# Kernel optimization log

Measured on AMD Instinct MI355X. Metric: run time of the kernel, lower is better.

The kernel has to match this reference:

```python
import jax, jax.numpy as jnp
import numpy as np
from jax import lax


def conv_valid_relu(x, w, b):
    # NHWC valid conv, stride 1, + bias + relu (matches keras Conv2D(..., activation='relu'))
    y = lax.conv_general_dilated(x, w, (1, 1), 'VALID',
                                 dimension_numbers=('NHWC', 'HWIO', 'NHWC'))
    return jax.nn.relu(y + b)


def maxpool2(x):
    # keras MaxPooling2D(): pool 2x2, stride 2, VALID
    return lax.reduce_window(x, -jnp.inf, lax.max, (1, 2, 2, 1), (1, 2, 2, 1), 'VALID')


def affine_bilinear(img, theta):
    # img: [H, W, C]; theta: [6] = (a0..a5).
    # tf.raw_ops.ImageProjectiveTransformV3 semantics (a6=a7=0):
    #   x_in = a0*x_out + a1*y_out + a2;  y_in = a3*x_out + a4*y_out + a5
    # BILINEAR interp; each of the 4 neighbor reads returns fill_value(=0) if out of bounds.
    H, W, C = img.shape
    a0, a1, a2, a3, a4, a5 = theta
    ys, xs = jnp.meshgrid(jnp.arange(H, dtype=img.dtype),
                          jnp.arange(W, dtype=img.dtype), indexing='ij')
    xq = a0 * xs + a1 * ys + a2  # [H, W]
    yq = a3 * xs + a4 * ys + a5
    x0 = jnp.floor(xq)
    y0 = jnp.floor(yq)
    dx = xq - x0
    dy = yq - y0

    def read(yi, xi):
        valid = (yi >= 0) & (yi <= H - 1) & (xi >= 0) & (xi <= W - 1)
        yc = jnp.clip(yi, 0, H - 1).astype(jnp.int32)
        xc = jnp.clip(xi, 0, W - 1).astype(jnp.int32)
        v = img[yc, xc]  # gather -> [H, W, C]
        return jnp.where(valid[..., None], v, jnp.zeros((), img.dtype))

    v00 = read(y0, x0)
    v01 = read(y0, x0 + 1)
    v10 = read(y0 + 1, x0)
    v11 = read(y0 + 1, x0 + 1)
    top = v00 * (1 - dx)[..., None] + v01 * dx[..., None]
    bot = v10 * (1 - dx)[..., None] + v11 * dx[..., None]
    return top * (1 - dy)[..., None] + bot * dy[..., None]


def reference(x, conv1_w, conv1_b, conv2_w, conv2_b, fc_w, fc_b):
    y = conv_valid_relu(x, conv1_w, conv1_b)   # [B,218,218,8]
    y = maxpool2(y)                            # [B,109,109,8]
    y = conv_valid_relu(y, conv2_w, conv2_b)   # [B,105,105,10]
    y = maxpool2(y)                            # [B,52,52,10]
    feat = y.reshape(y.shape[0], -1)           # row-major HWC flatten == keras Flatten
    theta = feat @ fc_w + fc_b                 # [B,6]
    return jax.vmap(affine_bilinear)(x, theta)


def setup_inputs() -> dict:
    key = jax.random.key(0)
    ks = jax.random.split(key, 6)
    B, H, W, C = 64, 224, 224, 3
    flat_dim = 52 * 52 * 10  # from 224 -> conv7 -> pool -> conv5 -> pool
    x = jax.random.normal(ks[0], (B, H, W, C), dtype=jnp.float32)
    conv1_w = jax.random.normal(ks[1], (7, 7, 3, 8), dtype=jnp.float32) * 0.05
    conv1_b = jnp.zeros((8,), jnp.float32)
    conv2_w = jax.random.normal(ks[2], (5, 5, 8, 10), dtype=jnp.float32) * 0.05
    conv2_b = jnp.zeros((10,), jnp.float32)
    # keras init: kernel zeros, bias = identity affine. Add tiny noise to kernel so the
    # predicted transform actually varies per image (exercises the resampler).
    fc_w = jax.random.normal(ks[3], (flat_dim, 6), dtype=jnp.float32) * 1e-4
    fc_b = jnp.array([1.0, 0.0, 0.0, 0.0, 1.0, 0.0], dtype=jnp.float32)
    return {"x": x, "conv1_w": conv1_w, "conv1_b": conv1_b,
            "conv2_w": conv2_w, "conv2_b": conv2_b, "fc_w": fc_w, "fc_b": fc_b}
```

## Files before the change

### kernel.cpp

```cpp
#include <hip/hip_runtime.h>
#include <math.h>

#define BATCH 64
#define HI 224
#define WI 224
#define P1H 109
#define P1W 109
#define P2H 52
#define P2W 52

typedef _Float16 f16;
typedef _Float16 f16x4 __attribute__((ext_vector_type(4)));
typedef _Float16 f16x8 __attribute__((ext_vector_type(8)));
typedef float    f32x4 __attribute__((ext_vector_type(4)));

#define MFMA16F(a,b,c) __builtin_amdgcn_mfma_f32_16x16x32_f16((a),(b),(c),0,0,0)

#define PROWS 4
#define NROWG 28
#define SROWS 14
#define ROWSH 896
#define STOT  (SROWS*ROWSH)
#define SPAD  12576
__global__ __launch_bounds__(256) void conv1_kernel(
    const float* __restrict__ x, const float* __restrict__ w1,
    const float* __restrict__ b1,
    f16* __restrict__ p1)
{
    __shared__ f16 smem[SPAD + 7*16*32];
    f16* sh_a = smem;
    f16* sh_b = smem + SPAD;

    const int tid  = threadIdx.x;
    const int lane = tid & 63;
    const int wave = tid >> 6;
    const int bph  = blockIdx.x;
    const int b    = blockIdx.y;
    const int ph0  = PROWS*bph;
    const int ir0  = 2*ph0;

    for (int i = tid; i < 7*16*32; i += 256) sh_b[i] = (f16)0.f;
    __syncthreads();

    for (int i = tid; i < 1176; i += 256) {
        const float v = w1[i];
        const int co = i & 7;
        const int t3 = i >> 3;
        const int ci = t3 % 3;
        const int kk = t3 / 3;
        const int kh = kk / 7;
        const int kw = kk - kh*7;
        sh_b[(kh*16 + co)*32 + kw*4 + ci] = (f16)v;
    }

    for (int u = wave; u < 25; u += 4) {
        const int q = u*512 + lane*8;
        if (q >= SPAD) continue;
        const int row  = q / ROWSH;
        const int rem  = q - row*ROWSH;
        const int col0 = rem >> 2;
        const int ira  = ir0 + row;
        float f0=0.f,f1=0.f,f2=0.f,f3=0.f,f4=0.f,f5=0.f;
        if (q < STOT && ira < HI) {
            const float* src = x + ((size_t)(b*HI + ira)*WI + col0)*3;
            const float2 a = *(const float2*)(src);
            const float2 c = *(const float2*)(src+2);
            const float2 e = *(const float2*)(src+4);
            f0=a.x; f1=a.y; f2=c.x; f3=c.y; f4=e.x; f5=e.y;
        }
        f16x8 hv;
        hv[0]=(f16)f0; hv[1]=(f16)f1; hv[2]=(f16)f2; hv[3]=(f16)0.f;
        hv[4]=(f16)f3; hv[5]=(f16)f4; hv[6]=(f16)f5; hv[7]=(f16)0.f;
        *(f16x8*)(sh_a + q) = hv;
    }
    __syncthreads();

    const int n16 = lane & 15;
    const int g   = lane >> 4;

    f16x8 bw[7];
#pragma unroll
    for (int kh = 0; kh < 7; ++kh)
        bw[kh] = *(const f16x8*)(sh_b + (kh*16 + n16)*32 + g*8);
    const float bias = b1[n16 & 7];

    for (int t = wave; t < 14; t += 4) {
        const int abase = (t*16 + n16)*4 + g*8;
        f32x4 acc[8];
#pragma unroll
        for (int cr = 0; cr < 8; ++cr) acc[cr] = (f32x4){0.f,0.f,0.f,0.f};

#pragma unroll
        for (int ir = 0; ir < SROWS; ++ir) {
            const int sb = ir*ROWSH + abase;
            const int klo = (ir > 7) ? (ir-7) : 0;
            const int khi = (ir < 6) ? ir : 6;
            const f16x4 h0 = *(const f16x4*)(sh_a + sb);
            const f16x4 h1 = *(const f16x4*)(sh_a + sb + 4);
            const f16x8 ah = __builtin_shufflevector(h0,h1,0,1,2,3,4,5,6,7);
#pragma unroll
            for (int kh = klo; kh <= khi; ++kh)
                acc[ir-kh] = MFMA16F(ah, bw[kh], acc[ir-kh]);
        }

        if (n16 < 8) {
#pragma unroll
            for (int pr = 0; pr < PROWS; ++pr) {
                const int ph = ph0 + pr;
                if (ph >= P1H) break;
#pragma unroll
                for (int q = 0; q < 2; ++q) {
                    const int pc = t*8 + 2*g + q;
                    if (pc < P1W) {
                        float m = fmaxf(fmaxf(acc[2*pr][2*q], acc[2*pr][2*q+1]),
                                        fmaxf(acc[2*pr+1][2*q], acc[2*pr+1][2*q+1]));
                        m = fmaxf(m + bias, 0.f);
                        const size_t oi = ((size_t)((b*P1H + ph)*P1W) + pc)*8 + n16;
                        p1[oi] = (f16)m;
                    }
                }
            }
        }
    }
}

#define C2A 6144
__global__ __launch_bounds__(256) void conv2_kernel(
    const f16* __restrict__ p1,
    const float* __restrict__ w2, const float* __restrict__ b2,
    float* __restrict__ p2)
{
    __shared__ f16 smem[C2A + 16*224];
    f16* sh_a = smem;
    f16* sh_b = smem + C2A;

    const int tid = threadIdx.x;
    const int ph  = blockIdx.x;
    const int b   = blockIdx.y;

    for (int i = tid; i < 16*224; i += 256) sh_b[i] = (f16)0.f;
    for (int i = tid; i < C2A - 5232; i += 256) sh_a[5232 + i] = (f16)0.f;
    __syncthreads();

    for (int i = tid; i < 2000; i += 256) {
        const float v = w2[i];
        const int kh = i / 400;
        int rem = i - kh*400;
        const int kw = rem / 80;
        rem -= kw*80;
        const int ci = rem / 10;
        const int co = rem - ci*10;
        sh_b[co*224 + kh*40 + kw*8 + ci] = (f16)v;
    }

    const size_t gbase = ((size_t)b*P1H + 2*ph) * (P1W*8);
    const ulong2* gsrc = (const ulong2*)(p1 + gbase);
    ulong2* gdst = (ulong2*)sh_a;
    for (int c = tid; c < 654; c += 256) gdst[c] = gsrc[c];
    __syncthreads();

    const int lane = tid & 63;
    const int wave = tid >> 6;
    const int n16  = lane & 15;
    const int g    = lane >> 4;

    f16x8 bh[7];
#pragma unroll
    for (int j = 0; j < 7; ++j)
        bh[j] = *(const f16x8*)(sh_b + n16*224 + j*32 + g*8);
    const float bias = (n16 < 10) ? b2[n16] : 0.f;

    int koff[7];
#pragma unroll
    for (int j = 0; j < 7; ++j) {
        const int chunk = 4*j + g;
        const int kh = chunk / 5;
        const int kw = chunk - kh*5;
        koff[j] = kh*872 + kw*8;
    }

    for (int t = wave; t < 7; t += 4) {
        const int c0 = t*16;
        const int pbase = (c0 + n16)*8;
        float res[2][4];
#pragma unroll
        for (int ro = 0; ro < 2; ++ro) {
            f32x4 accA = {0.f,0.f,0.f,0.f};
            f32x4 accB = {0.f,0.f,0.f,0.f};
            const int rb = ro*872 + pbase;
#pragma unroll
            for (int j = 0; j < 7; ++j) {
                const int si = rb + koff[j];
                const f16x8 ah = *(const f16x8*)(sh_a + si);
                if (j & 1) accB = MFMA16F(ah, bh[j], accB);
                else       accA = MFMA16F(ah, bh[j], accA);
            }
#pragma unroll
            for (int r = 0; r < 4; ++r) res[ro][r] = accA[r] + accB[r];
        }
        if (n16 < 10) {
#pragma unroll
            for (int q = 0; q < 2; ++q) {
                const int pc = (c0 >> 1) + 2*g + q;
                if (pc < P2W) {
                    float m = fmaxf(fmaxf(res[0][2*q], res[0][2*q+1]),
                                    fmaxf(res[1][2*q], res[1][2*q+1]));
                    p2[((size_t)((b*P2H + ph)*P2W) + pc)*10 + n16] = fmaxf(m + bias, 0.f);
                }
            }
        }
    }
}

__global__ __launch_bounds__(256) void fcA_kernel(
    const float* __restrict__ p2, const float* __restrict__ fw,
    float* __restrict__ partial)
{
    const int s = blockIdx.x;
    const int b = blockIdx.y;
    const int base = s * 3380;
    const float* f = p2 + (size_t)b*27040;
    float acc[6] = {0.f,0.f,0.f,0.f,0.f,0.f};
    for (int i = threadIdx.x; i < 3380; i += 256) {
        const float v = f[base + i];
        const float* wp = fw + (size_t)(base + i)*6;
#pragma unroll
        for (int k = 0; k < 6; ++k) acc[k] = fmaf(v, wp[k], acc[k]);
    }
    __shared__ float red[4][6];
#pragma unroll
    for (int k = 0; k < 6; ++k) {
        float v = acc[k];
        for (int off = 32; off > 0; off >>= 1) v += __shfl_down(v, off);
        if ((threadIdx.x & 63) == 0) red[threadIdx.x >> 6][k] = v;
    }
    __syncthreads();
    if (threadIdx.x < 6) {
        const int k = threadIdx.x;
        partial[(b*8 + s)*6 + k] = red[0][k] + red[1][k] + red[2][k] + red[3][k];
    }
}

__global__ __launch_bounds__(384) void fcB_kernel(
    const float* __restrict__ partial, const float* __restrict__ fb,
    float* __restrict__ theta)
{
    const int t = threadIdx.x;
    const int b = t / 6, k = t - b*6;
    float s = fb[k];
#pragma unroll
    for (int j = 0; j < 8; ++j) s += partial[(b*8 + j)*6 + k];
    theta[b*6 + k] = s;
}

__global__ __launch_bounds__(256) void resample_kernel(
    const float* __restrict__ x, const float* __restrict__ theta,
    float* __restrict__ out)
{
    const int idx = blockIdx.x * 256 + threadIdx.x;
    const int total = BATCH * HI * WI;
    if (idx >= total) return;
    const int b   = idx / (HI*WI);
    const int pix = idx - b * (HI*WI);
    const int yo  = pix / WI;
    const int xo  = pix - yo * WI;

    const float* t = theta + b*6;
    const float a0 = t[0], a1 = t[1], a2 = t[2], a3 = t[3], a4 = t[4], a5 = t[5];

    const float fx = (float)xo, fy = (float)yo;
    const float xq = a0*fx + a1*fy + a2;
    const float yq = a3*fx + a4*fy + a5;
    const float x0f = floorf(xq), y0f = floorf(yq);
    const float dx = xq - x0f, dy = yq - y0f;
    const int x0 = (int)x0f, y0 = (int)y0f;

    const float* img = x + (size_t)b * (HI*WI*3);

    const int x1 = x0 + 1, y1 = y0 + 1;
    const bool vx0 = (x0 >= 0) && (x0 <= WI-1);
    const bool vx1 = (x1 >= 0) && (x1 <= WI-1);
    const bool vy0 = (y0 >= 0) && (y0 <= HI-1);
    const bool vy1 = (y1 >= 0) && (y1 <= HI-1);
    const int xc0 = min(max(x0, 0), WI-1);
    const int xc1 = min(max(x1, 0), WI-1);
    const int yc0 = min(max(y0, 0), HI-1);
    const int yc1 = min(max(y1, 0), HI-1);
    const float* p00 = img + (size_t)(yc0*WI + xc0)*3;
    const float* p01 = img + (size_t)(yc0*WI + xc1)*3;
    const float* p10 = img + (size_t)(yc1*WI + xc0)*3;
    const float* p11 = img + (size_t)(yc1*WI + xc1)*3;
    const float m00 = (vy0 && vx0) ? 1.f : 0.f;
    const float m01 = (vy0 && vx1) ? 1.f : 0.f;
    const float m10 = (vy1 && vx0) ? 1.f : 0.f;
    const float m11 = (vy1 && vx1) ? 1.f : 0.f;

    float* op = out + (size_t)idx * 3;
#pragma unroll
    for (int c = 0; c < 3; ++c) {
        const float v00 = m00 * p00[c];
        const float v01 = m01 * p01[c];
        const float v10 = m10 * p10[c];
        const float v11 = m11 * p11[c];
        const float top = v00 * (1.f - dx) + v01 * dx;
        const float bot = v10 * (1.f - dx) + v11 * dx;
        op[c] = top * (1.f - dy) + bot * dy;
    }
}

extern "C" void kernel_launch(void* const* d_in, const int* in_sizes, int n_in,
                              void* d_out, int out_size, void* d_ws, size_t ws_size,
                              hipStream_t stream) {
    const float* x   = (const float*)d_in[0];
    const float* w1  = (const float*)d_in[1];
    const float* b1  = (const float*)d_in[2];
    const float* w2  = (const float*)d_in[3];
    const float* b2  = (const float*)d_in[4];
    const float* fw  = (const float*)d_in[5];
    const float* fb  = (const float*)d_in[6];
    float* out = (float*)d_out;

    char* ws = (char*)d_ws;
    f16*  p1      = (f16*)ws;
    float* p2     = (float*)(ws + 12166144);
    float* partial= (float*)(ws + 19088384);
    float* th     = (float*)(ws + 19100672);

    conv1_kernel<<<dim3(NROWG, BATCH), 256, 0, stream>>>(x, w1, b1, p1);
    conv2_kernel<<<dim3(P2H, BATCH), 256, 0, stream>>>(p1, w2, b2, p2);
    fcA_kernel<<<dim3(8, BATCH), 256, 0, stream>>>(p2, fw, partial);
    fcB_kernel<<<dim3(1), 384, 0, stream>>>(partial, fb, th);

    const int total_pix = BATCH * HI * WI;
    resample_kernel<<<dim3((total_pix + 255)/256), 256, 0, stream>>>(x, th, out);
}
```

Measured before the change: 76.76 us.

## Pack two conv row offsets into MFMA N dimension and merge FC kernels

Conv1 now fills the unused upper 8 output columns of each 16-wide MFMA weight tile with the same weights shifted by one kernel row. Each accumulator then computes two adjacent conv rows at once, which roughly halves the MFMA count, and the vertical pool max is taken with a cross-lane shuffle. The two-stage FC reduction is also folded into one kernel per batch, removing a launch at the cost of less parallelism per image.

```diff
diff --git a/kernel.cpp b/kernel.cpp
--- a/kernel.cpp
+++ b/kernel.cpp
@@ -22,12 +22,13 @@
 #define ROWSH 896
 #define STOT  (SROWS*ROWSH)
 #define SPAD  12576
+#define NBVAR 8
 __global__ __launch_bounds__(256) void conv1_kernel(
     const float* __restrict__ x, const float* __restrict__ w1,
     const float* __restrict__ b1,
     f16* __restrict__ p1)
 {
-    __shared__ f16 smem[SPAD + 7*16*32];
+    __shared__ f16 smem[SPAD + NBVAR*16*32];
     f16* sh_a = smem;
     f16* sh_b = smem + SPAD;
 
@@ -39,7 +40,7 @@
     const int ph0  = PROWS*bph;
     const int ir0  = 2*ph0;
 
-    for (int i = tid; i < 7*16*32; i += 256) sh_b[i] = (f16)0.f;
+    for (int i = tid; i < NBVAR*16*32; i += 256) sh_b[i] = (f16)0.f;
     __syncthreads();
 
     for (int i = tid; i < 1176; i += 256) {
@@ -50,7 +51,9 @@
         const int kk = t3 / 3;
         const int kh = kk / 7;
         const int kw = kk - kh*7;
-        sh_b[(kh*16 + co)*32 + kw*4 + ci] = (f16)v;
+        const f16 val = (f16)v;
+        sh_b[(kh*16     + co  )*32 + kw*4 + ci] = val;
+        sh_b[((kh+1)*16 + co+8)*32 + kw*4 + ci] = val;
     }
 
     for (int u = wave; u < 25; u += 4) {
@@ -78,47 +81,46 @@
     const int n16 = lane & 15;
     const int g   = lane >> 4;
 
-    f16x8 bw[7];
-#pragma unroll
-    for (int kh = 0; kh < 7; ++kh)
-        bw[kh] = *(const f16x8*)(sh_b + (kh*16 + n16)*32 + g*8);
+    f16x8 bv[NBVAR];
+#pragma unroll
+    for (int v = 0; v < NBVAR; ++v)
+        bv[v] = *(const f16x8*)(sh_b + (v*16 + n16)*32 + g*8);
     const float bias = b1[n16 & 7];
 
     for (int t = wave; t < 14; t += 4) {
         const int abase = (t*16 + n16)*4 + g*8;
-        f32x4 acc[8];
-#pragma unroll
-        for (int cr = 0; cr < 8; ++cr) acc[cr] = (f32x4){0.f,0.f,0.f,0.f};
+        f32x4 acc[4];
+#pragma unroll
+        for (int q = 0; q < 4; ++q) acc[q] = (f32x4){0.f,0.f,0.f,0.f};
 
 #pragma unroll
         for (int ir = 0; ir < SROWS; ++ir) {
             const int sb = ir*ROWSH + abase;
-            const int klo = (ir > 7) ? (ir-7) : 0;
-            const int khi = (ir < 6) ? ir : 6;
             const f16x4 h0 = *(const f16x4*)(sh_a + sb);
             const f16x4 h1 = *(const f16x4*)(sh_a + sb + 4);
             const f16x8 ah = __builtin_shufflevector(h0,h1,0,1,2,3,4,5,6,7);
 #pragma unroll
-            for (int kh = klo; kh <= khi; ++kh)
-                acc[ir-kh] = MFMA16F(ah, bw[kh], acc[ir-kh]);
-        }
-
-        if (n16 < 8) {
-#pragma unroll
-            for (int pr = 0; pr < PROWS; ++pr) {
-                const int ph = ph0 + pr;
-                if (ph >= P1H) break;
-#pragma unroll
-                for (int q = 0; q < 2; ++q) {
-                    const int pc = t*8 + 2*g + q;
-                    if (pc < P1W) {
-                        float m = fmaxf(fmaxf(acc[2*pr][2*q], acc[2*pr][2*q+1]),
-                                        fmaxf(acc[2*pr+1][2*q], acc[2*pr+1][2*q+1]));
-                        m = fmaxf(m + bias, 0.f);
-                        const size_t oi = ((size_t)((b*P1H + ph)*P1W) + pc)*8 + n16;
-                        p1[oi] = (f16)m;
-                    }
-                }
+            for (int q = 0; q < 4; ++q) {
+                const int v = ir - 2*q;
+                if (v >= 0 && v < NBVAR)
+                    acc[q] = MFMA16F(ah, bv[v], acc[q]);
+            }
+        }
+
+#pragma unroll
+        for (int pr = 0; pr < PROWS; ++pr) {
+            const float h0 = fmaxf(acc[pr][0], acc[pr][1]);
+            const float h1 = fmaxf(acc[pr][2], acc[pr][3]);
+            const float v0 = fmaxf(h0, __shfl_xor(h0, 8));
+            const float v1 = fmaxf(h1, __shfl_xor(h1, 8));
+            const int ph = ph0 + pr;
+            if (n16 < 8 && ph < P1H) {
+                const int pc0 = t*8 + 2*g;
+                const size_t rbase = ((size_t)(b*P1H + ph))*P1W*8;
+                if (pc0 < P1W)
+                    p1[rbase + (size_t)pc0*8 + n16] = (f16)fmaxf(v0 + bias, 0.f);
+                if (pc0+1 < P1W)
+                    p1[rbase + (size_t)(pc0+1)*8 + n16] = (f16)fmaxf(v1 + bias, 0.f);
             }
         }
     }
@@ -212,18 +214,16 @@
     }
 }
 
-__global__ __launch_bounds__(256) void fcA_kernel(
+__global__ __launch_bounds__(256) void fc_kernel(
     const float* __restrict__ p2, const float* __restrict__ fw,
-    float* __restrict__ partial)
+    const float* __restrict__ fb, float* __restrict__ theta)
 {
-    const int s = blockIdx.x;
-    const int b = blockIdx.y;
-    const int base = s * 3380;
-    const float* f = p2 + (size_t)b*27040;
+    const int b = blockIdx.x;
+    const float* f = p2 + (size_t)b * 27040;
     float acc[6] = {0.f,0.f,0.f,0.f,0.f,0.f};
-    for (int i = threadIdx.x; i < 3380; i += 256) {
-        const float v = f[base + i];
-        const float* wp = fw + (size_t)(base + i)*6;
+    for (int i = threadIdx.x; i < 27040; i += 256) {
+        const float v = f[i];
+        const float* wp = fw + (size_t)i * 6;
 #pragma unroll
         for (int k = 0; k < 6; ++k) acc[k] = fmaf(v, wp[k], acc[k]);
     }
@@ -237,20 +237,8 @@
     __syncthreads();
     if (threadIdx.x < 6) {
         const int k = threadIdx.x;
-        partial[(b*8 + s)*6 + k] = red[0][k] + red[1][k] + red[2][k] + red[3][k];
-    }
-}
-
-__global__ __launch_bounds__(384) void fcB_kernel(
-    const float* __restrict__ partial, const float* __restrict__ fb,
-    float* __restrict__ theta)
-{
-    const int t = threadIdx.x;
-    const int b = t / 6, k = t - b*6;
-    float s = fb[k];
-#pragma unroll
-    for (int j = 0; j < 8; ++j) s += partial[(b*8 + j)*6 + k];
-    theta[b*6 + k] = s;
+        theta[b*6 + k] = red[0][k] + red[1][k] + red[2][k] + red[3][k] + fb[k];
+    }
 }
 
 __global__ __launch_bounds__(256) void resample_kernel(
@@ -323,13 +311,11 @@
     char* ws = (char*)d_ws;
     f16*  p1      = (f16*)ws;
     float* p2     = (float*)(ws + 12166144);
-    float* partial= (float*)(ws + 19088384);
-    float* th     = (float*)(ws + 19100672);
+    float* th     = (float*)(ws + 19088384);
 
     conv1_kernel<<<dim3(NROWG, BATCH), 256, 0, stream>>>(x, w1, b1, p1);
     conv2_kernel<<<dim3(P2H, BATCH), 256, 0, stream>>>(p1, w2, b2, p2);
-    fcA_kernel<<<dim3(8, BATCH), 256, 0, stream>>>(p2, fw, partial);
-    fcB_kernel<<<dim3(1), 384, 0, stream>>>(partial, fb, th);
+    fc_kernel<<<dim3(BATCH), 256, 0, stream>>>(p2, fw, fb, th);
 
     const int total_pix = BATCH * HI * WI;
     resample_kernel<<<dim3((total_pix + 255)/256), 256, 0, stream>>>(x, th, out);
```

New measurement: 97.74 us. +27.3%, slower.
